# Kernel tuning notes

Measured on AMD Instinct MI355X. Metric: run time of the kernel, lower is better.

Reference implementation:

```python
import jax, jax.numpy as jnp
import numpy as np

WS = 6      # window_size
SS = 3      # shift_size
NH = 8      # num_heads
DIM = 384
HD = DIM // NH
SCALE = HD ** -0.5


def _window_mask(H, W):
    # region ids: [:ss,:ss]=0, [:ss,ss:]=1, [ss:,:ss]=2, [ss:,ss:]=3
    row = (jnp.arange(H) >= SS).astype(jnp.int32)
    col = (jnp.arange(W) >= SS).astype(jnp.int32)
    region = row[:, None] * 2 + col[None, :]            # (H, W)
    region = jnp.roll(region, (-SS, -SS), axis=(0, 1))
    ids = region.reshape(H // WS, WS, W // WS, WS).transpose(0, 2, 1, 3)
    ids = ids.reshape(-1, WS * WS)                      # (nW, V)
    eq = ids[:, :, None] == ids[:, None, :]             # (nW, V, V)
    return jnp.where(eq, 0.0, -jnp.inf).astype(jnp.float32)


def setup_inputs():
    key = jax.random.key(0)
    k = jax.random.split(key, 5)
    B, H, W, D = 32, 48, 48, DIM
    return {
        "x": jax.random.normal(k[0], (B, H, W, D), jnp.float32),
        "w_qkv": jax.random.normal(k[1], (D, 3 * D), jnp.float32) * 0.02,
        "b_qkv": jax.random.normal(k[2], (3 * D,), jnp.float32) * 0.02,
        "w_proj": jax.random.normal(k[3], (D, D), jnp.float32) * 0.02,
        "b_proj": jax.random.normal(k[4], (D,), jnp.float32) * 0.02,
    }


def reference(x, w_qkv, b_qkv, w_proj, b_proj):
    B, H, W, D = x.shape
    nWh, nWw = H // WS, W // WS
    nW, V = nWh * nWw, WS * WS

    x = jnp.roll(x, (-SS, -SS), axis=(1, 2))
    amask = _window_mask(H, W)                          # (nW, V, V)

    # window partition -> (B*nW, V, D)
    xw = x.reshape(B, nWh, WS, nWw, WS, D).transpose(0, 1, 3, 2, 4, 5)
    xw = xw.reshape(B * nW, V, D)

    qkv = xw @ w_qkv + b_qkv                            # (M, V, 3D)
    qkv = qkv.reshape(B * nW, V, 3, NH, HD).transpose(2, 0, 3, 1, 4)
    q, k, v = qkv[0], qkv[1], qkv[2]                    # (M, NH, V, HD)

    scores = jnp.einsum("mhvd,mhud->mhvu", q, k) * SCALE
    scores = scores.reshape(B, nW, NH, V, V) + amask[None, :, None]
    attn = jax.nn.softmax(scores, axis=-1).reshape(B * nW, NH, V, V)

    out = jnp.einsum("mhvu,mhud->mhvd", attn, v)        # (M, NH, V, HD)
    out = out.transpose(0, 2, 1, 3).reshape(B * nW, V, D)

    # window reverse -> (B, H, W, D)
    out = out.reshape(B, nWh, nWw, WS, WS, D).transpose(0, 1, 3, 2, 4, 5)
    out = out.reshape(B, H, W, D)
    out = jnp.roll(out, (SS, SS), axis=(1, 2))
    return out @ w_proj + b_proj
```

## Files before the change

kernel.cpp:

```cpp
#include <hip/hip_runtime.h>
#include <hip/hip_bf16.h>

namespace {

constexpr int Bn   = 32;
constexpr int IMG  = 48;
constexpr int Dm   = 384;
constexpr int NHn  = 8;
constexpr int WSn  = 6;
constexpr int NWn  = 64;
constexpr int Mn   = Bn * NWn;
constexpr int Vn   = 36;
constexpr int ROWS = Mn * Vn;
constexpr int K3   = 3 * Dm;
constexpr int HEADS_E = Vn * 48;
constexpr float SCALE = 0.14433756729740643f;

using short8 = __attribute__((ext_vector_type(8))) short;
using f32x4  = __attribute__((ext_vector_type(4))) float;

__device__ __forceinline__ float bf2f(unsigned short u) {
    return __uint_as_float(((unsigned)u) << 16);
}
__device__ __forceinline__ unsigned short f2bf(float f) {
    unsigned u = __float_as_uint(f);
    u += 0x7FFFu + ((u >> 16) & 1u);
    return (unsigned short)(u >> 16);
}

__device__ __forceinline__ int invol(int f) {
    return (f & 56) | ((f ^ (f >> 3)) & 7);
}

__device__ __forceinline__ void gl_lds16(const unsigned short* g, unsigned short* l) {
    __builtin_amdgcn_global_load_lds(
        (const __attribute__((address_space(1))) unsigned int*)g,
        (__attribute__((address_space(3))) unsigned int*)l, 16, 0, 0);
}

__device__ __forceinline__ int gather_base(int row) {
    int m = row / Vn, v = row - m * Vn;
    int b = m >> 6, w = m & 63;
    int wh = w >> 3, ww = w & 7;
    int gh = wh * WSn + v / WSn;
    int gw = ww * WSn + v % WSn;
    int fi = (gh + 3) % IMG;
    int fj = (gw + 3) % IMG;
    return ((b * IMG + fi) * IMG + fj) * Dm;
}

__device__ __forceinline__ int region_id(int t, int wh, int ww) {
    int hi = (wh == 7) ? ((t / 6) < 3) : 1;
    int lo = (ww == 7) ? ((t % 6) < 3) : 1;
    return (hi << 1) | lo;
}

__global__ __launch_bounds__(256)
void gather_x(const float* __restrict__ x, unsigned short* __restrict__ xg)
{
    int idx = blockIdx.x * 256 + threadIdx.x;
    int row = idx / 96;
    int c4  = (idx - row * 96) * 4;
    float4 v = *(const float4*)(x + (size_t)gather_base(row) + c4);
    ushort4 o;
    o.x = f2bf(v.x); o.y = f2bf(v.y); o.z = f2bf(v.z); o.w = f2bf(v.w);
    *(ushort4*)(xg + (size_t)row * Dm + c4) = o;
}

__global__ __launch_bounds__(256)
void prep_w(const float* __restrict__ wq, const float* __restrict__ wp,
            unsigned short* __restrict__ wqT, unsigned short* __restrict__ wpT)
{
    int idx = blockIdx.x * 256 + threadIdx.x;
    if (idx < K3 * Dm) {
        int n = idx / Dm, k = idx - n * Dm;
        wqT[idx] = f2bf(wq[(size_t)k * K3 + n]);
    } else {
        int i2 = idx - K3 * Dm;
        if (i2 < Dm * Dm) {
            int n = i2 / Dm, k = i2 - n * Dm;
            wpT[i2] = f2bf(wp[(size_t)k * Dm + n]);
        }
    }
}

__global__ __launch_bounds__(256)
void qkv_mfma(const unsigned short* __restrict__ xg,
              const unsigned short* __restrict__ wqT,
              const float* __restrict__ bq,
              unsigned short* __restrict__ qh,
              unsigned short* __restrict__ kh,
              unsigned short* __restrict__ vh)
{
    __shared__ __align__(16) unsigned short As[2][128 * 32];
    __shared__ __align__(16) unsigned short Bs[2][128 * 32];

    const int tid  = threadIdx.x;
    const int wave = tid >> 6, lane = tid & 63;
    const int quad = lane >> 4, l15 = lane & 15;
    const int id = (blockIdx.x & 7) * 648 + (blockIdx.x >> 3);
    const int nT = id % (K3 / 128);
    const int mT = id / (K3 / 128);
    const int rowA0 = mT * 128, rowB0 = nT * 128;

    const int fS  = invol(lane);
    const int rS  = fS >> 2;
    const int kcS = (fS & 3) * 8;
    const unsigned short* gA = xg  + (size_t)(rowA0 + wave * 32 + rS) * Dm + kcS;
    const unsigned short* gB = wqT + (size_t)(rowB0 + wave * 32 + rS) * Dm + kcS;

    const int wm = wave >> 1, wn = wave & 1;
    int aoff[4], boff[4];
#pragma unroll
    for (int i = 0; i < 4; i++) {
        int R = wm * 64 + i * 16 + l15;
        aoff[i] = (R >> 4) * 512 + invol((R & 15) * 4 + quad) * 8;
        int S = wn * 64 + i * 16 + l15;
        boff[i] = (S >> 4) * 512 + invol((S & 15) * 4 + quad) * 8;
    }

    auto STAGE = [&](int buf, int k0) {
        gl_lds16(gA + k0,           &As[buf][(wave * 32) * 32]);
        gl_lds16(gA + 16 * Dm + k0, &As[buf][(wave * 32 + 16) * 32]);
        gl_lds16(gB + k0,           &Bs[buf][(wave * 32) * 32]);
        gl_lds16(gB + 16 * Dm + k0, &Bs[buf][(wave * 32 + 16) * 32]);
    };

    f32x4 acc[4][4];
#pragma unroll
    for (int i = 0; i < 4; i++)
#pragma unroll
        for (int j = 0; j < 4; j++) acc[i][j] = (f32x4){0.f, 0.f, 0.f, 0.f};

    STAGE(0, 0);
    __syncthreads();

    for (int k0 = 0; k0 < Dm; k0 += 32) {
        const int cur = (k0 >> 5) & 1;
        if (k0 + 32 < Dm) STAGE(cur ^ 1, k0 + 32);
        short8 af[4], bfr[4];
#pragma unroll
        for (int i = 0; i < 4; i++) af[i]  = *(const short8*)&As[cur][aoff[i]];
#pragma unroll
        for (int j = 0; j < 4; j++) bfr[j] = *(const short8*)&Bs[cur][boff[j]];
#pragma unroll
        for (int i = 0; i < 4; i++)
#pragma unroll
            for (int j = 0; j < 4; j++)
                acc[i][j] = __builtin_amdgcn_mfma_f32_16x16x32_bf16(af[i], bfr[j], acc[i][j], 0, 0, 0);
        if (k0 + 32 < Dm) __syncthreads();
    }

    unsigned short* outb = (nT < 3) ? qh : (nT < 6) ? kh : vh;
    const int csub = (nT < 3) ? 0 : (nT < 6) ? 384 : 768;
#pragma unroll
    for (int j = 0; j < 4; j++) {
        int col = rowB0 + wn * 64 + j * 16 + l15;
        float b = bq[col];
        int c  = col - csub;
        int hh = c / 48, dd = c - hh * 48;
#pragma unroll
        for (int i = 0; i < 4; i++) {
#pragma unroll
            for (int r = 0; r < 4; r++) {
                int row = rowA0 + wm * 64 + i * 16 + quad * 4 + r;
                int mm = row / 36, vv = row - mm * 36;
                outb[((size_t)(mm * 8 + hh) * 36 + vv) * 48 + dd] = f2bf(acc[i][j][r] + b);
            }
        }
    }
}

__global__ __launch_bounds__(256)
void attn_mfma(const unsigned short* __restrict__ qh,
               const unsigned short* __restrict__ kh,
               const unsigned short* __restrict__ vh,
               unsigned short* __restrict__ att)
{
    __shared__ __align__(16) unsigned short Pl[4][48 * 56];
    __shared__ __align__(16) unsigned short Vt[4][48 * 64];

    const int tid  = threadIdx.x;
    const int wave = tid >> 6, lane = tid & 63;
    const int quad = lane >> 4, l15 = lane & 15;
    const int W = blockIdx.x * 4 + wave;
    const int m = W >> 3, h = W & 7;
    const int w = m & 63, wh = w >> 3, ww = w & 7;
    const bool need_mask = (wh == 7) || (ww == 7);

    const short8 zf = {0, 0, 0, 0, 0, 0, 0, 0};

    {
        short8* vz = (short8*)&Vt[0][0];
#pragma unroll
        for (int z = 0; z < 6; z++) vz[z * 256 + tid] = zf;
    }
    __syncthreads();

    const size_t hb = (size_t)(m * 8 + h) * HEADS_E;

    const unsigned short* qb = qh + hb;
    const unsigned short* kb = kh + hb;
    short8 qf[3][2], kf[3][2];
#pragma unroll
    for (int t = 0; t < 3; t++) {
        const unsigned short* qr = qb + (t * 16 + l15) * 48;
        qf[t][0] = *(const short8*)(qr + quad * 8);
        qf[t][1] = (quad < 2) ? *(const short8*)(qr + 32 + quad * 8) : zf;
        const unsigned short* kr = kb + (t * 16 + l15) * 48;
        kf[t][0] = *(const short8*)(kr + quad * 8);
        kf[t][1] = *(const short8*)(kr + 32 + quad * 8);
    }

    unsigned short* vws = &Vt[wave][0];
    {
        const unsigned short* vb = vh + hb;
#pragma unroll
        for (int p = 0; p < 4; p++) {
            int c = p * 64 + lane;
            if (c < 216) {
                short8 vv = *(const short8*)(vb + c * 8);
                int v  = c / 6, d0 = (c - v * 6) * 8;
                int g  = v >> 3, v7 = v & 7;
#pragma unroll
                for (int jj = 0; jj < 8; jj++) {
                    int d = d0 + jj;
                    int slot = (g + (d & 7) + (d >> 3)) & 7;
                    vws[d * 64 + slot * 8 + v7] = (unsigned short)vv[jj];
                }
            }
        }
    }

    f32x4 acc[3][3];
#pragma unroll
    for (int i = 0; i < 3; i++)
#pragma unroll
        for (int j = 0; j < 3; j++) acc[i][j] = (f32x4){0.f, 0.f, 0.f, 0.f};
    __builtin_amdgcn_s_setprio(1);
#pragma unroll
    for (int i = 0; i < 3; i++)
#pragma unroll
        for (int j = 0; j < 3; j++) {
            acc[i][j] = __builtin_amdgcn_mfma_f32_16x16x32_bf16(qf[i][0], kf[j][0], acc[i][j], 0, 0, 0);
            acc[i][j] = __builtin_amdgcn_mfma_f32_16x16x32_bf16(qf[i][1], kf[j][1], acc[i][j], 0, 0, 0);
        }
    __builtin_amdgcn_s_setprio(0);

#pragma unroll
    for (int i = 0; i < 3; i++) {
        float rs[4] = {0.f, 0.f, 0.f, 0.f};
        if (need_mask) {
#pragma unroll
            for (int j = 0; j < 3; j++) {
                int C = j * 16 + l15;
                int idc = region_id(C, wh, ww);
#pragma unroll
                for (int r = 0; r < 4; r++) {
                    int R = i * 16 + quad * 4 + r;
                    int idr = region_id(R, wh, ww);
                    float s = acc[i][j][r] * SCALE;
                    s = (C >= 36 || idr != idc) ? -1e30f : fminf(s, 30.f);
                    float e = __expf(s);
                    acc[i][j][r] = e;
                    rs[r] += e;
                }
            }
        } else {
#pragma unroll
            for (int j = 0; j < 3; j++) {
                int C = j * 16 + l15;
#pragma unroll
                for (int r = 0; r < 4; r++) {
                    float s = acc[i][j][r] * SCALE;
                    s = (C >= 36) ? -1e30f : fminf(s, 30.f);
                    float e = __expf(s);
                    acc[i][j][r] = e;
                    rs[r] += e;
                }
            }
        }
#pragma unroll
        for (int r = 0; r < 4; r++) {
#pragma unroll
            for (int d = 1; d < 16; d <<= 1) rs[r] += __shfl_xor(rs[r], d, 16);
            rs[r] = 1.f / rs[r];
        }
#pragma unroll
        for (int j = 0; j < 3; j++)
#pragma unroll
            for (int r = 0; r < 4; r++) {
                int R = i * 16 + quad * 4 + r;
                int C = j * 16 + l15;
                Pl[wave][R * 56 + C] = f2bf(acc[i][j][r] * rs[r]);
            }
    }
    __syncthreads();

    short8 pf[3][2], vf[3][2];
#pragma unroll
    for (int t = 0; t < 3; t++) {
        const unsigned short* pr = &Pl[wave][(t * 16 + l15) * 56];
        pf[t][0] = *(const short8*)(pr + quad * 8);
        pf[t][1] = (quad < 2) ? *(const short8*)(pr + 32 + quad * 8) : zf;
        int d  = t * 16 + l15;
        int sb = (d & 7) + (d >> 3);
        vf[t][0] = *(const short8*)(vws + d * 64 + (((quad + sb) & 7) * 8));
        vf[t][1] = *(const short8*)(vws + d * 64 + (((quad + 4 + sb) & 7) * 8));
    }
    f32x4 oacc[3][3];
#pragma unroll
    for (int i = 0; i < 3; i++)
#pragma unroll
        for (int j = 0; j < 3; j++) oacc[i][j] = (f32x4){0.f, 0.f, 0.f, 0.f};
    __builtin_amdgcn_s_setprio(1);
#pragma unroll
    for (int i = 0; i < 3; i++)
#pragma unroll
        for (int j = 0; j < 3; j++) {
            oacc[i][j] = __builtin_amdgcn_mfma_f32_16x16x32_bf16(pf[i][0], vf[j][0], oacc[i][j], 0, 0, 0);
            oacc[i][j] = __builtin_amdgcn_mfma_f32_16x16x32_bf16(pf[i][1], vf[j][1], oacc[i][j], 0, 0, 0);
        }
    __builtin_amdgcn_s_setprio(0);

#pragma unroll
    for (int i = 0; i < 3; i++)
#pragma unroll
        for (int r = 0; r < 4; r++) {
            int R = i * 16 + quad * 4 + r;
            if (R < 36) {
#pragma unroll
                for (int j = 0; j < 3; j++)
                    att[((size_t)m * 36 + R) * Dm + h * 48 + j * 16 + l15] = f2bf(oacc[i][j][r]);
            }
        }
}

__global__ __launch_bounds__(256)
void proj_mfma(const unsigned short* __restrict__ att,
               const unsigned short* __restrict__ wpT,
               const float* __restrict__ bp,
               float* __restrict__ out)
{
    __shared__ __align__(16) unsigned short As[2][128 * 32];
    __shared__ __align__(16) unsigned short Bs[2][128 * 32];
    __shared__ int rowOut[128];

    const int tid  = threadIdx.x;
    const int wave = tid >> 6, lane = tid & 63;
    const int quad = lane >> 4, l15 = lane & 15;
    const int id = (blockIdx.x & 7) * 216 + (blockIdx.x >> 3);
    const int nT = id % (Dm / 128);
    const int mT = id / (Dm / 128);
    const int rowA0 = mT * 128, rowB0 = nT * 128;

    if (tid < 128) rowOut[tid] = gather_base(rowA0 + tid);

    const int fS  = invol(lane);
    const int rS  = fS >> 2;
    const int kcS = (fS & 3) * 8;
    const unsigned short* gA = att + (size_t)(rowA0 + wave * 32 + rS) * Dm + kcS;
    const unsigned short* gB = wpT + (size_t)(rowB0 + wave * 32 + rS) * Dm + kcS;

    const int wm = wave >> 1, wn = wave & 1;
    int aoff[4], boff[4];
#pragma unroll
    for (int i = 0; i < 4; i++) {
        int R = wm * 64 + i * 16 + l15;
        aoff[i] = (R >> 4) * 512 + invol((R & 15) * 4 + quad) * 8;
        int S = wn * 64 + i * 16 + l15;
        boff[i] = (S >> 4) * 512 + invol((S & 15) * 4 + quad) * 8;
    }

    auto STAGE = [&](int buf, int k0) {
        gl_lds16(gA + k0,           &As[buf][(wave * 32) * 32]);
        gl_lds16(gA + 16 * Dm + k0, &As[buf][(wave * 32 + 16) * 32]);
        gl_lds16(gB + k0,           &Bs[buf][(wave * 32) * 32]);
        gl_lds16(gB + 16 * Dm + k0, &Bs[buf][(wave * 32 + 16) * 32]);
    };

    f32x4 acc[4][4];
#pragma unroll
    for (int i = 0; i < 4; i++)
#pragma unroll
        for (int j = 0; j < 4; j++) acc[i][j] = (f32x4){0.f, 0.f, 0.f, 0.f};

    STAGE(0, 0);
    __syncthreads();

    for (int k0 = 0; k0 < Dm; k0 += 32) {
        const int cur = (k0 >> 5) & 1;
        if (k0 + 32 < Dm) STAGE(cur ^ 1, k0 + 32);
        short8 af[4], bfr[4];
#pragma unroll
        for (int i = 0; i < 4; i++) af[i]  = *(const short8*)&As[cur][aoff[i]];
#pragma unroll
        for (int j = 0; j < 4; j++) bfr[j] = *(const short8*)&Bs[cur][boff[j]];
#pragma unroll
        for (int i = 0; i < 4; i++)
#pragma unroll
            for (int j = 0; j < 4; j++)
                acc[i][j] = __builtin_amdgcn_mfma_f32_16x16x32_bf16(af[i], bfr[j], acc[i][j], 0, 0, 0);
        if (k0 + 32 < Dm) __syncthreads();
    }

#pragma unroll
    for (int j = 0; j < 4; j++) {
        int col = rowB0 + wn * 64 + j * 16 + l15;
        float b = bp[col];
#pragma unroll
        for (int i = 0; i < 4; i++) {
#pragma unroll
            for (int r = 0; r < 4; r++) {
                int lrow = wm * 64 + i * 16 + quad * 4 + r;
                out[(size_t)rowOut[lrow] + col] = acc[i][j][r] + b;
            }
        }
    }
}

}

extern "C" void kernel_launch(void* const* d_in, const int* in_sizes, int n_in,
                              void* d_out, int out_size, void* d_ws, size_t ws_size,
                              hipStream_t stream)
{
    const float* x  = (const float*)d_in[0];
    const float* wq = (const float*)d_in[1];
    const float* bq = (const float*)d_in[2];
    const float* wp = (const float*)d_in[3];
    const float* bp = (const float*)d_in[4];
    float* out = (float*)d_out;

    const size_t HE   = (size_t)Mn * NHn * HEADS_E;
    const size_t XG_E = (size_t)ROWS * Dm;
    unsigned short* qh  = (unsigned short*)d_ws;
    unsigned short* kh  = qh + HE;
    unsigned short* vh  = kh + HE;
    unsigned short* xg  = vh + HE;
    unsigned short* att = xg;
    unsigned short* wqT = xg + XG_E;
    unsigned short* wpT = wqT + (size_t)K3 * Dm;

    prep_w   <<<(K3 * Dm + Dm * Dm + 255) / 256, 256, 0, stream>>>(wq, wp, wqT, wpT);
    gather_x <<<ROWS * (Dm / 4) / 256,            256, 0, stream>>>(x, xg);
    qkv_mfma <<<(ROWS / 128) * (K3 / 128),        256, 0, stream>>>(xg, wqT, bq, qh, kh, vh);
    attn_mfma<<<(Mn * NHn) / 4,                   256, 0, stream>>>(qh, kh, vh, att);
    proj_mfma<<<(ROWS / 128) * (Dm / 128),        256, 0, stream>>>(att, wpT, bp, out);
}
```

Baseline: 421.3 us.

## Merge gather and weight-prep kernels; single-buffer LDS in GEMM kernels

New measurement: 409.4 us. 2.8% less time.

```diff
diff --git a/kernel.cpp b/kernel.cpp
--- a/kernel.cpp
+++ b/kernel.cpp
@@ -14,14 +14,13 @@
 constexpr int ROWS = Mn * Vn;
 constexpr int K3   = 3 * Dm;
 constexpr int HEADS_E = Vn * 48;
+constexpr int GATHER_BLOCKS = ROWS * (Dm / 4) / 256;
+constexpr int PREP_BLOCKS   = (K3 * Dm + Dm * Dm) / 256;
 constexpr float SCALE = 0.14433756729740643f;
 
 using short8 = __attribute__((ext_vector_type(8))) short;
 using f32x4  = __attribute__((ext_vector_type(4))) float;
 
-__device__ __forceinline__ float bf2f(unsigned short u) {
-    return __uint_as_float(((unsigned)u) << 16);
-}
 __device__ __forceinline__ unsigned short f2bf(float f) {
     unsigned u = __float_as_uint(f);
     u += 0x7FFFu + ((u >> 16) & 1u);
@@ -56,30 +55,30 @@
 }
 
 __global__ __launch_bounds__(256)
-void gather_x(const float* __restrict__ x, unsigned short* __restrict__ xg)
+void gather_prep(const float* __restrict__ x,
+                 const float* __restrict__ wq, const float* __restrict__ wp,
+                 unsigned short* __restrict__ xg,
+                 unsigned short* __restrict__ wqT, unsigned short* __restrict__ wpT)
 {
-    int idx = blockIdx.x * 256 + threadIdx.x;
-    int row = idx / 96;
-    int c4  = (idx - row * 96) * 4;
-    float4 v = *(const float4*)(x + (size_t)gather_base(row) + c4);
-    ushort4 o;
-    o.x = f2bf(v.x); o.y = f2bf(v.y); o.z = f2bf(v.z); o.w = f2bf(v.w);
-    *(ushort4*)(xg + (size_t)row * Dm + c4) = o;
-}
-
-__global__ __launch_bounds__(256)
-void prep_w(const float* __restrict__ wq, const float* __restrict__ wp,
-            unsigned short* __restrict__ wqT, unsigned short* __restrict__ wpT)
-{
-    int idx = blockIdx.x * 256 + threadIdx.x;
-    if (idx < K3 * Dm) {
-        int n = idx / Dm, k = idx - n * Dm;
-        wqT[idx] = f2bf(wq[(size_t)k * K3 + n]);
+    if (blockIdx.x < GATHER_BLOCKS) {
+        int idx = blockIdx.x * 256 + threadIdx.x;
+        int row = idx / 96;
+        int c4  = (idx - row * 96) * 4;
+        float4 v = *(const float4*)(x + (size_t)gather_base(row) + c4);
+        ushort4 o;
+        o.x = f2bf(v.x); o.y = f2bf(v.y); o.z = f2bf(v.z); o.w = f2bf(v.w);
+        *(ushort4*)(xg + (size_t)row * Dm + c4) = o;
     } else {
-        int i2 = idx - K3 * Dm;
-        if (i2 < Dm * Dm) {
-            int n = i2 / Dm, k = i2 - n * Dm;
-            wpT[i2] = f2bf(wp[(size_t)k * Dm + n]);
+        int idx = (blockIdx.x - GATHER_BLOCKS) * 256 + threadIdx.x;
+        if (idx < K3 * Dm) {
+            int n = idx / Dm, k = idx - n * Dm;
+            wqT[idx] = f2bf(wq[(size_t)k * K3 + n]);
+        } else {
+            int i2 = idx - K3 * Dm;
+            if (i2 < Dm * Dm) {
+                int n = i2 / Dm, k = i2 - n * Dm;
+                wpT[i2] = f2bf(wp[(size_t)k * Dm + n]);
+            }
         }
     }
 }
@@ -92,8 +91,8 @@
               unsigned short* __restrict__ kh,
               unsigned short* __restrict__ vh)
 {
-    __shared__ __align__(16) unsigned short As[2][128 * 32];
-    __shared__ __align__(16) unsigned short Bs[2][128 * 32];
+    __shared__ __align__(16) unsigned short As[128 * 32];
+    __shared__ __align__(16) unsigned short Bs[128 * 32];
 
     const int tid  = threadIdx.x;
     const int wave = tid >> 6, lane = tid & 63;
@@ -108,6 +107,10 @@
     const int kcS = (fS & 3) * 8;
     const unsigned short* gA = xg  + (size_t)(rowA0 + wave * 32 + rS) * Dm + kcS;
     const unsigned short* gB = wqT + (size_t)(rowB0 + wave * 32 + rS) * Dm + kcS;
+    unsigned short* lA0 = &As[(wave * 32) * 32];
+    unsigned short* lA1 = &As[(wave * 32 + 16) * 32];
+    unsigned short* lB0 = &Bs[(wave * 32) * 32];
+    unsigned short* lB1 = &Bs[(wave * 32 + 16) * 32];
 
     const int wm = wave >> 1, wn = wave & 1;
     int aoff[4], boff[4];
@@ -119,36 +122,29 @@
         boff[i] = (S >> 4) * 512 + invol((S & 15) * 4 + quad) * 8;
     }
 
-    auto STAGE = [&](int buf, int k0) {
-        gl_lds16(gA + k0,           &As[buf][(wave * 32) * 32]);
-        gl_lds16(gA + 16 * Dm + k0, &As[buf][(wave * 32 + 16) * 32]);
-        gl_lds16(gB + k0,           &Bs[buf][(wave * 32) * 32]);
-        gl_lds16(gB + 16 * Dm + k0, &Bs[buf][(wave * 32 + 16) * 32]);
-    };
-
     f32x4 acc[4][4];
 #pragma unroll
     for (int i = 0; i < 4; i++)
 #pragma unroll
         for (int j = 0; j < 4; j++) acc[i][j] = (f32x4){0.f, 0.f, 0.f, 0.f};
 
-    STAGE(0, 0);
-    __syncthreads();
-
     for (int k0 = 0; k0 < Dm; k0 += 32) {
-        const int cur = (k0 >> 5) & 1;
-        if (k0 + 32 < Dm) STAGE(cur ^ 1, k0 + 32);
+        __syncthreads();
+        gl_lds16(gA + k0, lA0);
+        gl_lds16(gA + 16 * Dm + k0, lA1);
+        gl_lds16(gB + k0, lB0);
+        gl_lds16(gB + 16 * Dm + k0, lB1);
+        __syncthreads();
         short8 af[4], bfr[4];
 #pragma unroll
-        for (int i = 0; i < 4; i++) af[i]  = *(const short8*)&As[cur][aoff[i]];
-#pragma unroll
-        for (int j = 0; j < 4; j++) bfr[j] = *(const short8*)&Bs[cur][boff[j]];
+        for (int i = 0; i < 4; i++) af[i]  = *(const short8*)&As[aoff[i]];
+#pragma unroll
+        for (int j = 0; j < 4; j++) bfr[j] = *(const short8*)&Bs[boff[j]];
 #pragma unroll
         for (int i = 0; i < 4; i++)
 #pragma unroll
             for (int j = 0; j < 4; j++)
                 acc[i][j] = __builtin_amdgcn_mfma_f32_16x16x32_bf16(af[i], bfr[j], acc[i][j], 0, 0, 0);
-        if (k0 + 32 < Dm) __syncthreads();
     }
 
     unsigned short* outb = (nT < 3) ? qh : (nT < 6) ? kh : vh;
@@ -342,8 +338,8 @@
                const float* __restrict__ bp,
                float* __restrict__ out)
 {
-    __shared__ __align__(16) unsigned short As[2][128 * 32];
-    __shared__ __align__(16) unsigned short Bs[2][128 * 32];
+    __shared__ __align__(16) unsigned short As[128 * 32];
+    __shared__ __align__(16) unsigned short Bs[128 * 32];
     __shared__ int rowOut[128];
 
     const int tid  = threadIdx.x;
@@ -361,6 +357,10 @@
     const int kcS = (fS & 3) * 8;
     const unsigned short* gA = att + (size_t)(rowA0 + wave * 32 + rS) * Dm + kcS;
     const unsigned short* gB = wpT + (size_t)(rowB0 + wave * 32 + rS) * Dm + kcS;
+    unsigned short* lA0 = &As[(wave * 32) * 32];
+    unsigned short* lA1 = &As[(wave * 32 + 16) * 32];
+    unsigned short* lB0 = &Bs[(wave * 32) * 32];
+    unsigned short* lB1 = &Bs[(wave * 32 + 16) * 32];
 
     const int wm = wave >> 1, wn = wave & 1;
     int aoff[4], boff[4];
@@ -372,36 +372,29 @@
         boff[i] = (S >> 4) * 512 + invol((S & 15) * 4 + quad) * 8;
     }
 
-    auto STAGE = [&](int buf, int k0) {
-        gl_lds16(gA + k0,           &As[buf][(wave * 32) * 32]);
-        gl_lds16(gA + 16 * Dm + k0, &As[buf][(wave * 32 + 16) * 32]);
-        gl_lds16(gB + k0,           &Bs[buf][(wave * 32) * 32]);
-        gl_lds16(gB + 16 * Dm + k0, &Bs[buf][(wave * 32 + 16) * 32]);
-    };
-
     f32x4 acc[4][4];
 #pragma unroll
     for (int i = 0; i < 4; i++)
 #pragma unroll
         for (int j = 0; j < 4; j++) acc[i][j] = (f32x4){0.f, 0.f, 0.f, 0.f};
 
-    STAGE(0, 0);
-    __syncthreads();
-
     for (int k0 = 0; k0 < Dm; k0 += 32) {
-        const int cur = (k0 >> 5) & 1;
-        if (k0 + 32 < Dm) STAGE(cur ^ 1, k0 + 32);
+        __syncthreads();
+        gl_lds16(gA + k0, lA0);
+        gl_lds16(gA + 16 * Dm + k0, lA1);
+        gl_lds16(gB + k0, lB0);
+        gl_lds16(gB + 16 * Dm + k0, lB1);
+        __syncthreads();
         short8 af[4], bfr[4];
 #pragma unroll
-        for (int i = 0; i < 4; i++) af[i]  = *(const short8*)&As[cur][aoff[i]];
-#pragma unroll
-        for (int j = 0; j < 4; j++) bfr[j] = *(const short8*)&Bs[cur][boff[j]];
+        for (int i = 0; i < 4; i++) af[i]  = *(const short8*)&As[aoff[i]];
+#pragma unroll
+        for (int j = 0; j < 4; j++) bfr[j] = *(const short8*)&Bs[boff[j]];
 #pragma unroll
         for (int i = 0; i < 4; i++)
 #pragma unroll
             for (int j = 0; j < 4; j++)
                 acc[i][j] = __builtin_amdgcn_mfma_f32_16x16x32_bf16(af[i], bfr[j], acc[i][j], 0, 0, 0);
-        if (k0 + 32 < Dm) __syncthreads();
     }
 
 #pragma unroll
@@ -442,9 +435,8 @@
     unsigned short* wqT = xg + XG_E;
     unsigned short* wpT = wqT + (size_t)K3 * Dm;
 
-    prep_w   <<<(K3 * Dm + Dm * Dm + 255) / 256, 256, 0, stream>>>(wq, wp, wqT, wpT);
-    gather_x <<<ROWS * (Dm / 4) / 256,            256, 0, stream>>>(x, xg);
-    qkv_mfma <<<(ROWS / 128) * (K3 / 128),        256, 0, stream>>>(xg, wqT, bq, qh, kh, vh);
-    attn_mfma<<<(Mn * NHn) / 4,                   256, 0, stream>>>(qh, kh, vh, att);
-    proj_mfma<<<(ROWS / 128) * (Dm / 128),        256, 0, stream>>>(att, wpT, bp, out);
-}
+    gather_prep<<<GATHER_BLOCKS + PREP_BLOCKS, 256, 0, stream>>>(x, wq, wp, xg, wqT, wpT);
+    qkv_mfma   <<<(ROWS / 128) * (K3 / 128),   256, 0, stream>>>(xg, wqT, bq, qh, kh, vh);
+    attn_mfma  <<<(Mn * NHn) / 4,              256, 0, stream>>>(qh, kh, vh, att);
+    proj_mfma  <<<(ROWS / 128) * (Dm / 128),   256, 0, stream>>>(att, wpT, bp, out);
+}
```
